# Kernel tuning notes

Hardware: AMD Instinct MI355X
Metric: run time of the kernel (lower is better)

Reference implementation:

```python
import jax, jax.numpy as jnp
import numpy as np

R, C, M, G, H, W, NUM_POS = 2048, 81, 28, 100, 512, 512, 512


def roi_align_1s(feats, bidx, boxes, Mo):
    """RoI align with 1 sample per bin (bin center), spatial_scale=1.0, aligned=False.
    feats: [G,H,W]; bidx: [R] int (which feat map per roi); boxes: [R,4] (x1,y1,x2,y2).
    Returns [R,Mo,Mo]."""
    Hh, Ww = feats.shape[-2], feats.shape[-1]
    x1, y1, x2, y2 = boxes[:, 0], boxes[:, 1], boxes[:, 2], boxes[:, 3]
    grid = (jnp.arange(Mo, dtype=boxes.dtype) + 0.5) / Mo  # bin centers in [0,1)
    gx = x1[:, None] + grid[None, :] * (x2 - x1)[:, None]  # [R,Mo]
    gy = y1[:, None] + grid[None, :] * (y2 - y1)[:, None]  # [R,Mo]
    x = gx[:, None, :]  # [R,1,Mo]
    y = gy[:, :, None]  # [R,Mo,1]
    valid = (x > -1.0) & (x < Ww) & (y > -1.0) & (y < Hh)  # [R,Mo,Mo]
    xc = jnp.clip(x, 0.0, Ww - 1.0)
    yc = jnp.clip(y, 0.0, Hh - 1.0)
    x0 = jnp.floor(xc).astype(jnp.int32)
    y0 = jnp.floor(yc).astype(jnp.int32)
    x1i = jnp.minimum(x0 + 1, Ww - 1)
    y1i = jnp.minimum(y0 + 1, Hh - 1)
    lx = xc - x0
    ly = yc - y0
    b = bidx[:, None, None]
    v00 = feats[b, y0, x0]
    v01 = feats[b, y0, x1i]
    v10 = feats[b, y1i, x0]
    v11 = feats[b, y1i, x1i]
    val = (v00 * (1.0 - ly) * (1.0 - lx) + v01 * (1.0 - ly) * lx
           + v10 * ly * (1.0 - lx) + v11 * ly * lx)
    return jnp.where(valid, val, 0.0)


def setup_inputs() -> dict:
    key = jax.random.key(0)
    ks = jax.random.split(key, 8)
    class_logit = jax.random.normal(ks[0], (R, C), jnp.float32)
    box_regression = jax.random.normal(ks[1], (R, 4 * C), jnp.float32)
    regression_target = jax.random.normal(ks[2], (NUM_POS, 4), jnp.float32)
    mask_logit = jax.random.normal(ks[3], (R, C, M, M), jnp.float32)
    u = jax.random.uniform(ks[4], (R, 4), jnp.float32)
    bx1 = u[:, 0] * (W - 96.0)
    by1 = u[:, 1] * (H - 96.0)
    proposal = jnp.stack([bx1, by1, bx1 + 16.0 + u[:, 2] * 64.0, by1 + 16.0 + u[:, 3] * 64.0], axis=1)
    matched_idx = jax.random.randint(ks[5], (R,), 0, G)
    label = jax.random.randint(ks[6], (R,), 0, C)
    gt_mask = (jax.random.uniform(ks[7], (G, H, W)) > 0.5).astype(jnp.float32)
    return dict(class_logit=class_logit, box_regression=box_regression,
                regression_target=regression_target, mask_logit=mask_logit,
                proposal=proposal, gt_mask=gt_mask, matched_idx=matched_idx,
                label=label, num_pos=NUM_POS)


def reference(class_logit, box_regression, regression_target, mask_logit,
              proposal, gt_mask, matched_idx, label, num_pos):
    N = class_logit.shape[0]
    num_gt = gt_mask.shape[0]
    # ---- fastrcnn_loss ----
    logp = jax.nn.log_softmax(class_logit, axis=-1)
    cls_loss = -jnp.take_along_axis(logp, label[:, None], axis=1).mean()
    breg = box_regression.reshape(N, -1, 4)[:num_pos]          # [P, C, 4]
    pred = breg[jnp.arange(num_pos), label[:num_pos]]          # [P, 4]
    d = jnp.abs(pred - regression_target)
    box_loss = jnp.where(d < 1.0, 0.5 * d * d, d - 0.5).sum() / N  # smooth_l1(sum)/N
    # ---- maskrcnn_loss_average_per_gt ----
    Mo = mask_logit.shape[-1]
    mask_target = roi_align_1s(gt_mask, matched_idx, proposal, Mo)   # [N,M,M]
    sel = mask_logit[jnp.arange(N), label]                            # [N,M,M]
    # stable BCE-with-logits, reduction='none'
    bce = jnp.maximum(sel, 0.0) - sel * mask_target + jnp.log1p(jnp.exp(-jnp.abs(sel)))
    per_roi = bce.mean(axis=(-2, -1))                                 # [N]
    seg_sum = jax.ops.segment_sum(per_roi, matched_idx, num_segments=num_gt)
    cnt = jax.ops.segment_sum(jnp.ones_like(per_roi), matched_idx, num_segments=num_gt)
    per_gt = jnp.where(cnt > 0, seg_sum / jnp.maximum(cnt, 1.0), 0.0)  # [G]
    return jnp.concatenate([cls_loss[None], box_loss[None], per_gt])   # [2+G]
```

## Files before the change

### kernel.cpp

```cpp
#include <hip/hip_runtime.h>
#include <hip/hip_bf16.h>

#define RR 2048
#define CC 81
#define MM 28
#define GG 100
#define HH 512
#define WW 512

__global__ void init_kernel(float* out, float* ws) {
    int t = threadIdx.x;
    for (int i = t; i < 102; i += blockDim.x) out[i] = 0.0f;
    for (int i = t; i < 2 * GG; i += blockDim.x) ws[i] = 0.0f;
}

__global__ void cls_kernel(const float* __restrict__ logits,
                           const int* __restrict__ label,
                           float* __restrict__ out) {
    int wave = threadIdx.x >> 6;
    int lane = threadIdx.x & 63;
    int row = blockIdx.x * 4 + wave;
    if (row >= RR) return;

    const float* rowp = logits + (size_t)row * CC;
    float v0 = (lane < CC) ? rowp[lane] : -1e30f;
    float v1 = (lane + 64 < CC) ? rowp[lane + 64] : -1e30f;
    float m = fmaxf(v0, v1);
    #pragma unroll
    for (int off = 32; off > 0; off >>= 1) m = fmaxf(m, __shfl_down(m, off));
    m = __shfl(m, 0);

    float s = 0.0f;
    if (lane < CC) s += __expf(v0 - m);
    if (lane + 64 < CC) s += __expf(v1 - m);
    #pragma unroll
    for (int off = 32; off > 0; off >>= 1) s += __shfl_down(s, off);

    if (lane == 0) {
        float lse = m + __logf(s);
        float v = rowp[label[row]];
        atomicAdd(out + 0, (lse - v) * (1.0f / (float)RR));
    }
}

__global__ void box_kernel(const float* __restrict__ box_reg,
                           const float* __restrict__ reg_tgt,
                           const int* __restrict__ label,
                           const int* __restrict__ num_pos_p,
                           float* __restrict__ out) {
    int num_pos = *num_pos_p;
    int t = blockIdx.x * blockDim.x + threadIdx.x;
    float l = 0.0f;
    int i = t >> 2, j = t & 3;
    if (i < num_pos) {
        float pred = box_reg[(size_t)i * (4 * CC) + label[i] * 4 + j];
        float d = fabsf(pred - reg_tgt[i * 4 + j]);
        l = (d < 1.0f) ? 0.5f * d * d : d - 0.5f;
    }
    #pragma unroll
    for (int off = 32; off > 0; off >>= 1) l += __shfl_down(l, off);
    __shared__ float sm[8];
    int lane = threadIdx.x & 63, wid = threadIdx.x >> 6;
    if (lane == 0) sm[wid] = l;
    __syncthreads();
    if (threadIdx.x == 0) {
        float tot = 0.0f;
        int nw = blockDim.x >> 6;
        for (int k = 0; k < nw; k++) tot += sm[k];
        atomicAdd(out + 1, tot * (1.0f / (float)RR));
    }
}

__global__ void mask_kernel(const float* __restrict__ mask_logit,
                            const float* __restrict__ proposal,
                            const float* __restrict__ gt_mask,
                            const int* __restrict__ matched_idx,
                            const int* __restrict__ label,
                            float* __restrict__ seg_sum,
                            float* __restrict__ cnt) {
    int r = blockIdx.x;
    int t = threadIdx.x;

    float x1 = proposal[r * 4 + 0];
    float y1 = proposal[r * 4 + 1];
    float x2 = proposal[r * 4 + 2];
    float y2 = proposal[r * 4 + 3];
    int m_idx = matched_idx[r];
    int lbl = label[r];

    const float* sel = mask_logit + ((size_t)r * CC + lbl) * (MM * MM);
    const float* fm = gt_mask + (size_t)m_idx * (HH * WW);

    float bw = x2 - x1, bh = y2 - y1;

    float acc = 0.0f;
    for (int p = t; p < MM * MM; p += blockDim.x) {
        int py = p / MM, px = p % MM;
        float gx = x1 + ((px + 0.5f) / (float)MM) * bw;
        float gy = y1 + ((py + 0.5f) / (float)MM) * bh;
        bool valid = (gx > -1.0f) && (gx < (float)WW) && (gy > -1.0f) && (gy < (float)HH);
        float xc = fminf(fmaxf(gx, 0.0f), (float)(WW - 1));
        float yc = fminf(fmaxf(gy, 0.0f), (float)(HH - 1));
        int x0 = (int)floorf(xc);
        int y0 = (int)floorf(yc);
        int x1i = min(x0 + 1, WW - 1);
        int y1i = min(y0 + 1, HH - 1);
        float lx = xc - (float)x0;
        float ly = yc - (float)y0;
        float v00 = fm[y0 * WW + x0];
        float v01 = fm[y0 * WW + x1i];
        float v10 = fm[y1i * WW + x0];
        float v11 = fm[y1i * WW + x1i];
        float val = v00 * (1.0f - ly) * (1.0f - lx) + v01 * (1.0f - ly) * lx +
                    v10 * ly * (1.0f - lx) + v11 * ly * lx;
        float tgt = valid ? val : 0.0f;

        float s = sel[p];
        float bce = fmaxf(s, 0.0f) - s * tgt + log1pf(__expf(-fabsf(s)));
        acc += bce;
    }

    #pragma unroll
    for (int off = 32; off > 0; off >>= 1) acc += __shfl_down(acc, off);
    __shared__ float sm[8];
    int lane = t & 63, wid = t >> 6;
    if (lane == 0) sm[wid] = acc;
    __syncthreads();
    if (t == 0) {
        float tot = 0.0f;
        int nw = blockDim.x >> 6;
        for (int k = 0; k < nw; k++) tot += sm[k];
        float per_roi = tot * (1.0f / (float)(MM * MM));
        atomicAdd(seg_sum + m_idx, per_roi);
        atomicAdd(cnt + m_idx, 1.0f);
    }
}

__global__ void fin_kernel(const float* __restrict__ seg_sum,
                           const float* __restrict__ cnt,
                           float* __restrict__ out) {
    int g = threadIdx.x + blockIdx.x * blockDim.x;
    if (g < GG) {
        float c = cnt[g];
        out[2 + g] = (c > 0.0f) ? seg_sum[g] / fmaxf(c, 1.0f) : 0.0f;
    }
}

extern "C" void kernel_launch(void* const* d_in, const int* in_sizes, int n_in,
                              void* d_out, int out_size, void* d_ws, size_t ws_size,
                              hipStream_t stream) {
    const float* class_logit    = (const float*)d_in[0];
    const float* box_regression = (const float*)d_in[1];
    const float* regression_tgt = (const float*)d_in[2];
    const float* mask_logit     = (const float*)d_in[3];
    const float* proposal       = (const float*)d_in[4];
    const float* gt_mask        = (const float*)d_in[5];
    const int*   matched_idx    = (const int*)d_in[6];
    const int*   label          = (const int*)d_in[7];
    const int*   num_pos        = (const int*)d_in[8];

    float* out = (float*)d_out;
    float* seg_sum = (float*)d_ws;
    float* cnt = seg_sum + GG;

    init_kernel<<<1, 256, 0, stream>>>(out, seg_sum);

    cls_kernel<<<RR / 4, 256, 0, stream>>>(class_logit, label, out);

    box_kernel<<<(512 * 4 + 255) / 256, 256, 0, stream>>>(
        box_regression, regression_tgt, label, num_pos, out);

    mask_kernel<<<RR, 256, 0, stream>>>(mask_logit, proposal, gt_mask,
                                        matched_idx, label, seg_sum, cnt);

    fin_kernel<<<1, 128, 0, stream>>>(seg_sum, cnt, out);
}
```

Baseline: 652.0 us.

## Fuse cls, box and mask loss kernels into one wave-per-RoI kernel

Merges the classification, box regression and mask kernels into a single launch in which each 64-lane wave handles one RoI. The mask logits are read as float4 and reduced with wave shuffles only, replacing the shared-memory block reduction. This removes two kernel launches and the block-level sync. In exchange each RoI's 784 pixels are now processed by 64 lanes instead of 256 threads, so there is less parallelism per RoI.

```diff
diff --git a/kernel.cpp b/kernel.cpp
--- a/kernel.cpp
+++ b/kernel.cpp
@@ -14,125 +14,104 @@
     for (int i = t; i < 2 * GG; i += blockDim.x) ws[i] = 0.0f;
 }
 
-__global__ void cls_kernel(const float* __restrict__ logits,
-                           const int* __restrict__ label,
-                           float* __restrict__ out) {
-    int wave = threadIdx.x >> 6;
+__global__ __launch_bounds__(256) void fused_kernel(
+    const float* __restrict__ class_logit,
+    const float* __restrict__ box_reg,
+    const float* __restrict__ reg_tgt,
+    const float* __restrict__ mask_logit,
+    const float* __restrict__ proposal,
+    const float* __restrict__ gt_mask,
+    const int* __restrict__ matched_idx,
+    const int* __restrict__ label,
+    const int* __restrict__ num_pos_p,
+    float* __restrict__ out,
+    float* __restrict__ seg_sum,
+    float* __restrict__ cnt) {
     int lane = threadIdx.x & 63;
-    int row = blockIdx.x * 4 + wave;
-    if (row >= RR) return;
+    int r = blockIdx.x * 4 + (threadIdx.x >> 6);
 
-    const float* rowp = logits + (size_t)row * CC;
-    float v0 = (lane < CC) ? rowp[lane] : -1e30f;
-    float v1 = (lane + 64 < CC) ? rowp[lane + 64] : -1e30f;
-    float m = fmaxf(v0, v1);
-    #pragma unroll
-    for (int off = 32; off > 0; off >>= 1) m = fmaxf(m, __shfl_down(m, off));
-    m = __shfl(m, 0);
+    int lbl = label[r];
+    int m_idx = matched_idx[r];
 
-    float s = 0.0f;
-    if (lane < CC) s += __expf(v0 - m);
-    if (lane + 64 < CC) s += __expf(v1 - m);
-    #pragma unroll
-    for (int off = 32; off > 0; off >>= 1) s += __shfl_down(s, off);
-
-    if (lane == 0) {
-        float lse = m + __logf(s);
-        float v = rowp[label[row]];
-        atomicAdd(out + 0, (lse - v) * (1.0f / (float)RR));
-    }
-}
-
-__global__ void box_kernel(const float* __restrict__ box_reg,
-                           const float* __restrict__ reg_tgt,
-                           const int* __restrict__ label,
-                           const int* __restrict__ num_pos_p,
-                           float* __restrict__ out) {
     int num_pos = *num_pos_p;
-    int t = blockIdx.x * blockDim.x + threadIdx.x;
-    float l = 0.0f;
-    int i = t >> 2, j = t & 3;
-    if (i < num_pos) {
-        float pred = box_reg[(size_t)i * (4 * CC) + label[i] * 4 + j];
-        float d = fabsf(pred - reg_tgt[i * 4 + j]);
-        l = (d < 1.0f) ? 0.5f * d * d : d - 0.5f;
-    }
-    #pragma unroll
-    for (int off = 32; off > 0; off >>= 1) l += __shfl_down(l, off);
-    __shared__ float sm[8];
-    int lane = threadIdx.x & 63, wid = threadIdx.x >> 6;
-    if (lane == 0) sm[wid] = l;
-    __syncthreads();
-    if (threadIdx.x == 0) {
-        float tot = 0.0f;
-        int nw = blockDim.x >> 6;
-        for (int k = 0; k < nw; k++) tot += sm[k];
-        atomicAdd(out + 1, tot * (1.0f / (float)RR));
-    }
-}
-
-__global__ void mask_kernel(const float* __restrict__ mask_logit,
-                            const float* __restrict__ proposal,
-                            const float* __restrict__ gt_mask,
-                            const int* __restrict__ matched_idx,
-                            const int* __restrict__ label,
-                            float* __restrict__ seg_sum,
-                            float* __restrict__ cnt) {
-    int r = blockIdx.x;
-    int t = threadIdx.x;
-
-    float x1 = proposal[r * 4 + 0];
-    float y1 = proposal[r * 4 + 1];
-    float x2 = proposal[r * 4 + 2];
-    float y2 = proposal[r * 4 + 3];
-    int m_idx = matched_idx[r];
-    int lbl = label[r];
-
-    const float* sel = mask_logit + ((size_t)r * CC + lbl) * (MM * MM);
-    const float* fm = gt_mask + (size_t)m_idx * (HH * WW);
-
-    float bw = x2 - x1, bh = y2 - y1;
-
-    float acc = 0.0f;
-    for (int p = t; p < MM * MM; p += blockDim.x) {
-        int py = p / MM, px = p % MM;
-        float gx = x1 + ((px + 0.5f) / (float)MM) * bw;
-        float gy = y1 + ((py + 0.5f) / (float)MM) * bh;
-        bool valid = (gx > -1.0f) && (gx < (float)WW) && (gy > -1.0f) && (gy < (float)HH);
-        float xc = fminf(fmaxf(gx, 0.0f), (float)(WW - 1));
-        float yc = fminf(fmaxf(gy, 0.0f), (float)(HH - 1));
-        int x0 = (int)floorf(xc);
-        int y0 = (int)floorf(yc);
-        int x1i = min(x0 + 1, WW - 1);
-        int y1i = min(y0 + 1, HH - 1);
-        float lx = xc - (float)x0;
-        float ly = yc - (float)y0;
-        float v00 = fm[y0 * WW + x0];
-        float v01 = fm[y0 * WW + x1i];
-        float v10 = fm[y1i * WW + x0];
-        float v11 = fm[y1i * WW + x1i];
-        float val = v00 * (1.0f - ly) * (1.0f - lx) + v01 * (1.0f - ly) * lx +
-                    v10 * ly * (1.0f - lx) + v11 * ly * lx;
-        float tgt = valid ? val : 0.0f;
-
-        float s = sel[p];
-        float bce = fmaxf(s, 0.0f) - s * tgt + log1pf(__expf(-fabsf(s)));
-        acc += bce;
+    if (r < num_pos) {
+        float bl = 0.0f;
+        if (lane < 4) {
+            float pred = box_reg[(size_t)r * (4 * CC) + lbl * 4 + lane];
+            float d = fabsf(pred - reg_tgt[r * 4 + lane]);
+            bl = (d < 1.0f) ? 0.5f * d * d : d - 0.5f;
+        }
+        bl += __shfl_down(bl, 2);
+        bl += __shfl_down(bl, 1);
+        if (lane == 0) atomicAdd(out + 1, bl * (1.0f / (float)RR));
     }
 
-    #pragma unroll
-    for (int off = 32; off > 0; off >>= 1) acc += __shfl_down(acc, off);
-    __shared__ float sm[8];
-    int lane = t & 63, wid = t >> 6;
-    if (lane == 0) sm[wid] = acc;
-    __syncthreads();
-    if (t == 0) {
-        float tot = 0.0f;
-        int nw = blockDim.x >> 6;
-        for (int k = 0; k < nw; k++) tot += sm[k];
-        float per_roi = tot * (1.0f / (float)(MM * MM));
-        atomicAdd(seg_sum + m_idx, per_roi);
-        atomicAdd(cnt + m_idx, 1.0f);
+    {
+        const float* rowp = class_logit + (size_t)r * CC;
+        float v0 = (lane < CC) ? rowp[lane] : -1e30f;
+        float v1 = (lane + 64 < CC) ? rowp[lane + 64] : -1e30f;
+        float m = fmaxf(v0, v1);
+        #pragma unroll
+        for (int off = 32; off > 0; off >>= 1) m = fmaxf(m, __shfl_down(m, off));
+        m = __shfl(m, 0);
+        float s = 0.0f;
+        if (lane < CC) s += __expf(v0 - m);
+        if (lane + 64 < CC) s += __expf(v1 - m);
+        #pragma unroll
+        for (int off = 32; off > 0; off >>= 1) s += __shfl_down(s, off);
+        if (lane == 0) {
+            float lse = m + __logf(s);
+            atomicAdd(out + 0, (lse - rowp[lbl]) * (1.0f / (float)RR));
+        }
+    }
+
+    {
+        float x1 = proposal[r * 4 + 0];
+        float y1 = proposal[r * 4 + 1];
+        float x2 = proposal[r * 4 + 2];
+        float y2 = proposal[r * 4 + 3];
+        float bw = x2 - x1, bh = y2 - y1;
+
+        const float4* sel4 = (const float4*)(mask_logit + ((size_t)r * CC + lbl) * (MM * MM));
+        const float* fm = gt_mask + (size_t)m_idx * (HH * WW);
+
+        float acc = 0.0f;
+        for (int i4 = lane; i4 < (MM * MM) / 4; i4 += 64) {
+            float4 sv = sel4[i4];
+            float svv[4] = {sv.x, sv.y, sv.z, sv.w};
+            int pbase = i4 * 4;
+            #pragma unroll
+            for (int j = 0; j < 4; j++) {
+                int p = pbase + j;
+                int py = p / MM, px = p - py * MM;
+                float gx = x1 + ((px + 0.5f) / (float)MM) * bw;
+                float gy = y1 + ((py + 0.5f) / (float)MM) * bh;
+                bool valid = (gx > -1.0f) && (gx < (float)WW) && (gy > -1.0f) && (gy < (float)HH);
+                float xc = fminf(fmaxf(gx, 0.0f), (float)(WW - 1));
+                float yc = fminf(fmaxf(gy, 0.0f), (float)(HH - 1));
+                int x0 = (int)floorf(xc);
+                int y0 = (int)floorf(yc);
+                int x1i = min(x0 + 1, WW - 1);
+                int y1i = min(y0 + 1, HH - 1);
+                float lx = xc - (float)x0;
+                float ly = yc - (float)y0;
+                float v00 = fm[y0 * WW + x0];
+                float v01 = fm[y0 * WW + x1i];
+                float v10 = fm[y1i * WW + x0];
+                float v11 = fm[y1i * WW + x1i];
+                float val = v00 * (1.0f - ly) * (1.0f - lx) + v01 * (1.0f - ly) * lx +
+                            v10 * ly * (1.0f - lx) + v11 * ly * lx;
+                float tgt = valid ? val : 0.0f;
+                float s = svv[j];
+                acc += fmaxf(s, 0.0f) - s * tgt + log1pf(__expf(-fabsf(s)));
+            }
+        }
+        #pragma unroll
+        for (int off = 32; off > 0; off >>= 1) acc += __shfl_down(acc, off);
+        if (lane == 0) {
+            atomicAdd(seg_sum + m_idx, acc * (1.0f / (float)(MM * MM)));
+            atomicAdd(cnt + m_idx, 1.0f);
+        }
     }
 }
 
@@ -165,13 +144,9 @@
 
     init_kernel<<<1, 256, 0, stream>>>(out, seg_sum);
 
-    cls_kernel<<<RR / 4, 256, 0, stream>>>(class_logit, label, out);
-
-    box_kernel<<<(512 * 4 + 255) / 256, 256, 0, stream>>>(
-        box_regression, regression_tgt, label, num_pos, out);
-
-    mask_kernel<<<RR, 256, 0, stream>>>(mask_logit, proposal, gt_mask,
-                                        matched_idx, label, seg_sum, cnt);
+    fused_kernel<<<RR / 4, 256, 0, stream>>>(
+        class_logit, box_regression, regression_tgt, mask_logit, proposal,
+        gt_mask, matched_idx, label, num_pos, out, seg_sum, cnt);
 
     fin_kernel<<<1, 128, 0, stream>>>(seg_sum, cnt, out);
 }
```

New measurement: 646.0 us. About the same (-0.9%).
